# Performance work log

Hardware: AMD Instinct MI355X
Metric: run time of the kernel (lower is better)

The kernel has to match this reference:

```python
import jax, jax.numpy as jnp
from jax import lax
import numpy as np

NPOINT = 1024
RADII = (0.1, 0.2, 0.4)
NSAMPLES = (16, 32, 64)
MLPS = ((64, 64, 128), (128, 128, 256), (128, 128, 256))
IN_CH = 64  # 3 (xyz) + 61 (point features)
EPS = 1e-5


def setup_inputs() -> dict:
    key = jax.random.key(0)
    ks = jax.random.split(key, 64)
    inp = {
        "xyz": jax.random.normal(ks[0], (8, 3, 16384), dtype=jnp.float32),
        "points": jax.random.normal(ks[1], (8, 61, 16384), dtype=jnp.float32),
    }
    ki = 2
    for i, mlp in enumerate(MLPS):
        last = IN_CH
        for j, out_ch in enumerate(mlp):
            inp[f"w{i}{j}"] = jax.random.normal(ks[ki], (out_ch, last), dtype=jnp.float32) * 0.05
            inp[f"b{i}{j}"] = jnp.zeros((out_ch,), dtype=jnp.float32)
            inp[f"g{i}{j}"] = jnp.ones((out_ch,), dtype=jnp.float32)
            inp[f"bt{i}{j}"] = jnp.zeros((out_ch,), dtype=jnp.float32)
            last = out_ch
            ki += 1
    return inp


def square_distance(src, dst):
    # src [B,S,3], dst [B,N,3] -> [B,S,N]
    d = -2.0 * jnp.einsum("bsc,bnc->bsn", src, dst)
    d = d + jnp.sum(src * src, -1)[:, :, None]
    d = d + jnp.sum(dst * dst, -1)[:, None, :]
    return d


def farthest_point_sample(xyz, npoint):
    # xyz [B,N,3] -> idx [B,npoint]; deterministic start at index 0
    B, N, _ = xyz.shape
    def step(carry, _):
        distance, farthest = carry
        centroid = jnp.take_along_axis(xyz, farthest[:, None, None], axis=1)  # [B,1,3]
        dist = jnp.sum((xyz - centroid) ** 2, axis=-1)  # [B,N]
        distance = jnp.minimum(distance, dist)
        return (distance, jnp.argmax(distance, axis=-1).astype(jnp.int32)), farthest
    init = (jnp.full((B, N), 1e10, dtype=xyz.dtype), jnp.zeros((B,), dtype=jnp.int32))
    _, idxs = lax.scan(step, init, None, length=npoint)
    return idxs.T  # [B,npoint]


def gather_points(p, idx):
    # p [B,N,C], idx [B,...] -> [B,...,C]
    B = p.shape[0]
    flat = idx.reshape(B, -1)
    g = jnp.take_along_axis(p, flat[:, :, None], axis=1)
    return g.reshape(idx.shape + (p.shape[-1],))


def query_ball_points(radius, nsample, xyz, new_xyz):
    # xyz [B,N,3], new_xyz [B,S,3] -> idx [B,S,nsample]
    B, N, _ = xyz.shape
    d = square_distance(new_xyz, xyz)  # [B,S,N]
    idx = jnp.broadcast_to(jnp.arange(N, dtype=jnp.int32), d.shape)
    idx = jnp.where(d > radius * radius, N, idx)
    idx = jnp.sort(idx, axis=-1)[:, :, :nsample]
    first = idx[:, :, :1]
    return jnp.where(idx == N, first, idx)


def _forward(xyz, points, params):
    xyz_t = jnp.transpose(xyz, (0, 2, 1))       # [B,N,3]
    pts_t = jnp.transpose(points, (0, 2, 1))    # [B,N,D]
    B, N, _ = xyz_t.shape
    fps_idx = farthest_point_sample(xyz_t, NPOINT)
    new_xyz = gather_points(xyz_t, fps_idx)     # [B,S,3]
    feats = []
    for i, (radius, K) in enumerate(zip(RADII, NSAMPLES)):
        gidx = query_ball_points(radius, K, xyz_t, new_xyz)      # [B,S,K]
        grouped_xyz = gather_points(xyz_t, gidx) - new_xyz[:, :, None, :]
        grouped_pts = gather_points(pts_t, gidx)
        x = jnp.concatenate([grouped_xyz, grouped_pts], axis=-1)  # [B,S,K,IN_CH]
        for (w, b, g, bt) in params[i]:
            x = jnp.einsum("bskc,oc->bsko", x, w) + b  # 1x1 conv
            mean = jnp.mean(x, axis=(0, 1, 2))
            var = jnp.var(x, axis=(0, 1, 2))
            x = jax.nn.relu(g * (x - mean) * lax.rsqrt(var + EPS) + bt)
        feats.append(jnp.max(x, axis=2))  # [B,S,Cout]
    new_points = jnp.transpose(jnp.concatenate(feats, axis=-1), (0, 2, 1))  # [B,640,S]
    return jnp.transpose(new_xyz, (0, 2, 1)), new_points


def reference(xyz, points,
              w00, b00, g00, bt00, w01, b01, g01, bt01, w02, b02, g02, bt02,
              w10, b10, g10, bt10, w11, b11, g11, bt11, w12, b12, g12, bt12,
              w20, b20, g20, bt20, w21, b21, g21, bt21, w22, b22, g22, bt22):
    params = [
        [(w00, b00, g00, bt00), (w01, b01, g01, bt01), (w02, b02, g02, bt02)],
        [(w10, b10, g10, bt10), (w11, b11, g11, bt11), (w12, b12, g12, bt12)],
        [(w20, b20, g20, bt20), (w21, b21, g21, bt21), (w22, b22, g22, bt22)],
    ]
    return _forward(xyz, points, params)
```

## Files before the change

kernel.cpp:

```cpp
#include <hip/hip_runtime.h>
#include <stdint.h>

#define BB 8
#define NN 16384
#define SS 1024

typedef unsigned short u16;
typedef float f32x4 __attribute__((ext_vector_type(4)));
typedef short short8v __attribute__((ext_vector_type(8)));
typedef unsigned short us4 __attribute__((ext_vector_type(4)));
typedef unsigned short us8 __attribute__((ext_vector_type(8)));

static __device__ __forceinline__ float bf2f(u16 u){
    union { uint32_t u; float f; } v; v.u = ((uint32_t)u) << 16; return v.f;
}
static __device__ __forceinline__ u16 f2bf(float f){
    union { float f; uint32_t u; } v; v.f = f;
    return (u16)((v.u + 0x7FFFu + ((v.u >> 16) & 1u)) >> 16);
}
static constexpr int cmax2(int a, int b){ return a > b ? a : b; }

#define LP 12288
#define SM_FPS (LP*3*4 + SS*4 + 8)

__global__ __launch_bounds__(1024) void pre_kernel(
        const float* __restrict__ xyz, const float* __restrict__ pts,
        float* __restrict__ ptsT, float* __restrict__ q, float* __restrict__ out_xyz,
        const float* __restrict__ w0, const float* __restrict__ w1, const float* __restrict__ w2,
        const float* __restrict__ w3, const float* __restrict__ w4, const float* __restrict__ w5,
        const float* __restrict__ w6, const float* __restrict__ w7, const float* __restrict__ w8,
        u16* __restrict__ wbf0, u16* __restrict__ wbf1, u16* __restrict__ wbf2){
#pragma clang fp contract(off)
    __shared__ __align__(16) char smem_raw[SM_FPS];
    int t = threadIdx.x;

    if (blockIdx.x >= 8){
        int bx = blockIdx.x - 8;
        if (bx < 2048){
            float (*tile)[65] = (float (*)[65])smem_raw;
            int b = bx >> 8;
            int n0 = (bx & 255) * 64;
            int ln = t & 63, cr = t >> 6;
            for (int c = cr; c < 64; c += 16){
                float v;
                if (c < 3) v = xyz[((size_t)b*3 + c)*NN + n0 + ln];
                else       v = pts[((size_t)b*61 + (c-3))*NN + n0 + ln];
                tile[ln][c] = v;
            }
            __syncthreads();
            int lc = t & 63, nr = t >> 6;
            for (int n = nr; n < 64; n += 16){
                ptsT[((size_t)b*NN + n0 + n)*64 + lc] = tile[n][lc];
            }
        } else {
            int br = bx - 2048;
            const float* A; const float* B; const float* C; u16* out; int na, nb2, nc;
            if (br == 0){ A=w0; na=4096;  B=w1; nb2=4096;  C=w2; nc=8192;  out=wbf0; }
            else if (br == 1){ A=w3; na=8192; B=w4; nb2=16384; C=w5; nc=32768; out=wbf1; }
            else { A=w6; na=8192; B=w7; nb2=16384; C=w8; nc=32768; out=wbf2; }
            int tot = na + nb2 + nc;
            for (int i = t; i < tot; i += 1024){
                float v;
                if (i < na) v = A[i];
                else if (i < na+nb2) v = B[i-na];
                else v = C[i-na-nb2];
                out[i] = f2bf(v);
            }
        }
        return;
    }

    float* lx = (float*)smem_raw;
    float* ly = lx + LP;
    float* lz = ly + LP;
    int*  hist = (int*)(lz + LP);
    unsigned long long* slotp = (unsigned long long*)(hist + SS);
    int b = blockIdx.x;
    const float* xb = xyz + (size_t)b*3*NN;
    float px[16], py[16], pz[16], dd[16];
#pragma unroll
    for (int j=0;j<16;++j){
        int n = t + j*1024;
        px[j] = xb[n];
        py[j] = xb[NN+n];
        pz[j] = xb[2*NN+n];
        dd[j] = 1e10f;
    }
#pragma unroll
    for (int j=0;j<16;++j){
        asm volatile("" : "+v"(px[j]), "+v"(py[j]), "+v"(pz[j]));
    }
    for (int idx = t; idx < LP; idx += 1024){
        lx[idx] = xb[idx];
        ly[idx] = xb[NN+idx];
        lz[idx] = xb[2*NN+idx];
    }
    if (t == 0) *slotp = 0ull;
    __syncthreads();

    int lane = t & 63;
    int far = 0;
    float cx = xb[0], cy = xb[NN], cz = xb[2*NN];
    for (int it=0; it<SS; ++it){
        if (t==0) hist[it] = far;
#pragma unroll
        for (int j=0;j<16;++j){
            float dx = px[j]-cx, dy = py[j]-cy, dz = pz[j]-cz;
            float d = dx*dx + dy*dy;
            d = d + dz*dz;
            dd[j] = fminf(dd[j], d);
        }
        float m01 = fmaxf(dd[0], dd[1]),  m23 = fmaxf(dd[2], dd[3]);
        float m45 = fmaxf(dd[4], dd[5]),  m67 = fmaxf(dd[6], dd[7]);
        float m89 = fmaxf(dd[8], dd[9]),  mab = fmaxf(dd[10], dd[11]);
        float mcd = fmaxf(dd[12], dd[13]), mef = fmaxf(dd[14], dd[15]);
        float ma = fmaxf(fmaxf(m01, m23), fmaxf(m45, m67));
        float mb = fmaxf(fmaxf(m89, mab), fmaxf(mcd, mef));
        float mx = fmaxf(ma, mb);
        int bj = 0;
#pragma unroll
        for (int j=15; j>=0; --j){
            if (dd[j] == mx) bj = j;
        }
        int bn = t + (bj << 10);
        unsigned long long pk = ((unsigned long long)(unsigned)(it+1) << 46)
                              | ((unsigned long long)__float_as_uint(mx) << 14)
                              | (unsigned long long)(unsigned)(16383 - bn);
#pragma unroll
        for (int off=32; off>0; off>>=1){
            unsigned long long o = __shfl_down(pk, off);
            pk = (o > pk) ? o : pk;
        }
        if (lane == 0) atomicMax(slotp, pk);
        __syncthreads();
        unsigned long long win = *slotp;
        far = 16383 - (int)(win & 0x3FFFull);
        if (far < LP){
            cx = lx[far]; cy = ly[far]; cz = lz[far];
        } else {
            cx = xb[far]; cy = xb[NN+far]; cz = xb[2*NN+far];
        }
    }
    __syncthreads();
    {
        int s = t;
        int fidx = hist[s];
        float vx, vy, vz;
        if (fidx < LP){ vx = lx[fidx]; vy = ly[fidx]; vz = lz[fidx]; }
        else { vx = xb[fidx]; vy = xb[NN+fidx]; vz = xb[2*NN+fidx]; }
        int gi = b*SS + s;
        q[gi*3+0] = vx; q[gi*3+1] = vy; q[gi*3+2] = vz;
        out_xyz[((size_t)b*3+0)*SS + s] = vx;
        out_xyz[((size_t)b*3+1)*SS + s] = vy;
        out_xyz[((size_t)b*3+2)*SS + s] = vz;
    }
}

__global__ __launch_bounds__(256) void ballquery_kernel(const float* __restrict__ xyz, const float* __restrict__ q,
        int* __restrict__ idx0, int* __restrict__ idx1, int* __restrict__ idx2,
        float r2a, float r2b, float r2c){
#pragma clang fp contract(off)
    __shared__ int lds[4][112];
    int t = threadIdx.x;
    int w = t >> 6, lane = t & 63;
    int qi = blockIdx.x*4 + w;
    int b = qi >> 10;
    const float* xb = xyz + (size_t)b*3*NN;
    float qx = q[qi*3], qy = q[qi*3+1], qz = q[qi*3+2];
    float qn = qx*qx + qy*qy; qn = qn + qz*qz;
    int* l0 = lds[w];
    int* l1 = l0 + 16;
    int* l2 = l0 + 48;
    l0[lane] = 0;
    if (lane < 48) l0[64+lane] = 0;
    int c0=0, c1=0, c2=0;
    uint64_t below = (1ull << lane) - 1ull;
    for (int ch=0; ch<256; ++ch){
        int n = ch*64 + lane;
        float x = xb[n], y = xb[NN+n], z = xb[2*NN+n];
        float dn = x*x + y*y; dn = dn + z*z;
        float dot = qx*x + qy*y; dot = dot + qz*z;
        float d = -2.0f*dot + qn;
        d = d + dn;
        bool o0 = d <= r2a, o1 = d <= r2b, o2 = d <= r2c;
        uint64_t m0 = __ballot(o0), m1 = __ballot(o1), m2 = __ballot(o2);
        if (c0 < 16){
            int p = c0 + (int)__popcll(m0 & below);
            if (o0 && p < 16) l0[p] = n;
            c0 += (int)__popcll(m0); if (c0 > 16) c0 = 16;
        }
        if (c1 < 32){
            int p = c1 + (int)__popcll(m1 & below);
            if (o1 && p < 32) l1[p] = n;
            c1 += (int)__popcll(m1); if (c1 > 32) c1 = 32;
        }
        if (c2 < 64){
            int p = c2 + (int)__popcll(m2 & below);
            if (o2 && p < 64) l2[p] = n;
            c2 += (int)__popcll(m2); if (c2 > 64) c2 = 64;
        }
        if (c0>=16 && c1>=32 && c2>=64) break;
    }
    __syncthreads();
    int f0 = l0[0], f1 = l1[0], f2 = l2[0];
    if (lane >= c0 && lane < 16) l0[lane] = f0;
    if (lane >= c1 && lane < 32) l1[lane] = f1;
    if (lane >= c2)              l2[lane] = f2;
    __syncthreads();
    if (lane < 16) idx0[(size_t)qi*16 + lane] = l0[lane];
    if (lane < 32) idx1[(size_t)qi*32 + lane] = l1[lane];
    idx2[(size_t)qi*64 + lane] = l2[lane];
}


template<int CC, int OH>
__device__ __forceinline__ void load_W_frags(const u16* __restrict__ Wb,
                                             short8v (&wf)[CC/32][OH/64],
                                             int l, int w, int hoff){
    int rl = l & 15, kg = l >> 4;
#pragma unroll
    for (int ks=0; ks<CC/32; ++ks)
#pragma unroll
    for (int tc=0; tc<OH/64; ++tc){
        int col = hoff + w*(OH/4) + tc*16 + rl;
        wf[ks][tc] = *(const short8v*)(Wb + (size_t)col*CC + ks*32 + kg*8);
    }
}

template<int K>
__device__ __forceinline__ void stage_A_gather(const float* __restrict__ ptsT, const float* __restrict__ q,
                                               const int* __restrict__ gidx, int m0, int t, char* __restrict__ As){
    int r = t >> 2, q4 = t & 3;
    int m = m0 + r;
    int idx = gidx[m];
    int bs = m / K;
    int b = bs >> 10;
    const float* base = ptsT + ((size_t)b*NN + idx)*64;
    float qx=0.f, qy=0.f, qz=0.f;
    if (q4 == 0){ qx = q[bs*3]; qy = q[bs*3+1]; qz = q[bs*3+2]; }
    int rx = (r & 7) << 4;
#pragma unroll
    for (int ii=0; ii<4; ++ii){
        int c0 = q4*16 + ii*4;
        float4 v = *(const float4*)(base + c0);
        if (q4==0 && ii==0){ v.x -= qx; v.y -= qy; v.z -= qz; }
        us4 u;
        u[0]=f2bf(v.x); u[1]=f2bf(v.y); u[2]=f2bf(v.z); u[3]=f2bf(v.w);
        *(us4*)(As + r*128 + ((c0*2) ^ rx)) = u;
    }
}

template<int OP>
__device__ __forceinline__ void stage_A_z(const u16* __restrict__ zbuf, int m0,
                                          const float* __restrict__ sc, const float* __restrict__ sh,
                                          int t, char* __restrict__ As){
    constexpr int CQ = OP/4;
    for (int s = t; s < 64*CQ; s += 256){
        int r = s / CQ, cq = s - r*CQ;
        us4 zv = *(const us4*)&zbuf[((size_t)(m0+r))*OP + cq*4];
        int c = cq*4;
        us4 u;
        u[0] = f2bf(fmaxf(0.f, bf2f(zv[0])*sc[c+0] + sh[c+0]));
        u[1] = f2bf(fmaxf(0.f, bf2f(zv[1])*sc[c+1] + sh[c+1]));
        u[2] = f2bf(fmaxf(0.f, bf2f(zv[2])*sc[c+2] + sh[c+2]));
        u[3] = f2bf(fmaxf(0.f, bf2f(zv[3])*sc[c+3] + sh[c+3]));
        *(us4*)(As + r*(OP*2) + ((cq*8) ^ ((r&7)<<4))) = u;
    }
}

template<int CC, int OH>
__device__ __forceinline__ void mfma_gemm_v2(const char* __restrict__ As,
                                             const short8v (&wf)[CC/32][OH/64],
                                             f32x4 (&acc)[4][OH/64], int l){
    constexpr int CCB = CC*2;
    int rl = l & 15, kg = l >> 4;
    const char* ap = As + rl*CCB;
    int axor = (rl & 7) << 4;
#pragma unroll
    for (int ks=0; ks<CC/32; ++ks){
        int karg = ((ks<<6) | (kg<<4)) ^ axor;
        short8v a0 = *(const short8v*)(ap + 0*16*CCB + karg);
        short8v a1 = *(const short8v*)(ap + 1*16*CCB + karg);
        short8v a2 = *(const short8v*)(ap + 2*16*CCB + karg);
        short8v a3 = *(const short8v*)(ap + 3*16*CCB + karg);
#pragma unroll
        for (int tc=0; tc<OH/64; ++tc){
            acc[0][tc] = __builtin_amdgcn_mfma_f32_16x16x32_bf16(a0, wf[ks][tc], acc[0][tc], 0,0,0);
            acc[1][tc] = __builtin_amdgcn_mfma_f32_16x16x32_bf16(a1, wf[ks][tc], acc[1][tc], 0,0,0);
            acc[2][tc] = __builtin_amdgcn_mfma_f32_16x16x32_bf16(a2, wf[ks][tc], acc[2][tc], 0,0,0);
            acc[3][tc] = __builtin_amdgcn_mfma_f32_16x16x32_bf16(a3, wf[ks][tc], acc[3][tc], 0,0,0);
        }
    }
}

template<int OH>
__device__ __forceinline__ void bias_mfma(f32x4 (&acc)[4][OH/64], const float* __restrict__ bsrc,
                                          int l, int w, int coff){
#pragma unroll
    for (int tc=0; tc<OH/64; ++tc){
        float bb = bsrc[coff + w*(OH/4) + tc*16 + (l&15)];
#pragma unroll
        for (int tr=0; tr<4; ++tr)
#pragma unroll
        for (int e=0; e<4; ++e) acc[tr][tc][e] += bb;
    }
}

template<int OH, int OT>
__device__ __forceinline__ void zstore_mfma(f32x4 (&acc)[4][OH/64], u16* __restrict__ zbuf,
                                            int m0, int l, int w, int coff){
#pragma unroll
    for (int tr=0; tr<4; ++tr)
#pragma unroll
    for (int e=0; e<4; ++e){
        int row = tr*16 + (l>>4)*4 + e;
#pragma unroll
        for (int tc=0; tc<OH/64; ++tc){
            int c = coff + w*(OH/4) + tc*16 + (l&15);
            zbuf[((size_t)(m0+row))*OT + c] = f2bf(acc[tr][tc][e]);
        }
    }
}

template<int OH, int OT, int K, bool EXT>
__device__ __forceinline__ void stats_mfma(f32x4 (&acc)[4][OH/64], int l, int w, int m0, int blk, int coff,
    float* __restrict__ pS, float* __restrict__ pQ,
    float* __restrict__ gmax, float* __restrict__ gmin){
#pragma unroll
    for (int tc=0; tc<OH/64; ++tc){
        float s1 = 0.f, s2 = 0.f;
        float mxr[4], mnr[4];
#pragma unroll
        for (int tr=0; tr<4; ++tr){
            float v0=acc[tr][tc][0], v1=acc[tr][tc][1], v2=acc[tr][tc][2], v3=acc[tr][tc][3];
            s1 += (v0+v1)+(v2+v3);
            s2 += (v0*v0+v1*v1)+(v2*v2+v3*v3);
            if (EXT){
                mxr[tr] = fmaxf(fmaxf(v0,v1),fmaxf(v2,v3));
                mnr[tr] = fminf(fminf(v0,v1),fminf(v2,v3));
            }
        }
        s1 += __shfl_xor(s1,16); s1 += __shfl_xor(s1,32);
        s2 += __shfl_xor(s2,16); s2 += __shfl_xor(s2,32);
        if (EXT){
#pragma unroll
            for (int tr=0; tr<4; ++tr){
                mxr[tr] = fmaxf(mxr[tr], __shfl_xor(mxr[tr],16));
                mxr[tr] = fmaxf(mxr[tr], __shfl_xor(mxr[tr],32));
                mnr[tr] = fminf(mnr[tr], __shfl_xor(mnr[tr],16));
                mnr[tr] = fminf(mnr[tr], __shfl_xor(mnr[tr],32));
            }
        }
        if (l < 16){
            int c = coff + w*(OH/4) + tc*16 + l;
            pS[(size_t)blk*OT + c] = s1;
            pQ[(size_t)blk*OT + c] = s2;
            if (EXT){
                constexpr int G = 64/K, WG = K/16;
#pragma unroll
                for (int g=0; g<G; ++g){
                    float M1 = mxr[g*WG], M2 = mnr[g*WG];
#pragma unroll
                    for (int ww=1; ww<WG; ++ww){
                        M1 = fmaxf(M1, mxr[g*WG+ww]);
                        M2 = fminf(M2, mnr[g*WG+ww]);
                    }
                    gmax[(size_t)(m0/K + g)*OT + c] = M1;
                    gmin[(size_t)(m0/K + g)*OT + c] = M2;
                }
            }
        }
    }
}

template<int OH>
__device__ __forceinline__ void act_to_As_mfma(f32x4 (&acc)[4][OH/64], const float* __restrict__ bsrc,
    const float* __restrict__ sc, const float* __restrict__ sh, int l, int w, char* __restrict__ As){
#pragma unroll
    for (int tc=0; tc<OH/64; ++tc){
        int c = w*(OH/4) + tc*16 + (l&15);
        float bb = bsrc[c], scv = sc[c], shv = sh[c];
#pragma unroll
        for (int tr=0; tr<4; ++tr)
#pragma unroll
        for (int e=0; e<4; ++e){
            int row = tr*16 + (l>>4)*4 + e;
            float vv = fmaxf(0.f, (acc[tr][tc][e]+bb)*scv + shv);
            *(u16*)(As + row*(OH*2) + ((2*c) ^ ((row&7)<<4))) = f2bf(vv);
        }
    }
}

template<int PHASE, int K, int O1, int O2, int O3>
__global__ __launch_bounds__(256) void fused_mlp(
    const float* __restrict__ ptsT, const float* __restrict__ q, const int* __restrict__ gidx,
    const u16* __restrict__ Wb1, const float* __restrict__ b1,
    const u16* __restrict__ Wb2, const float* __restrict__ b2,
    const u16* __restrict__ Wb3, const float* __restrict__ b3,
    const float* __restrict__ sc1, const float* __restrict__ sh1,
    const float* __restrict__ sc2, const float* __restrict__ sh2,
    float* __restrict__ pS, float* __restrict__ pQ,
    float* __restrict__ gmax, float* __restrict__ gmin,
    u16* __restrict__ zbuf)
{
    constexpr int OH3 = (O3 > 128) ? 128 : O3;
    constexpr int AMX = (PHASE==1) ? 64 : (PHASE==2 ? O1 : (PHASE==3 ? cmax2(O1,O2) : O2));
    __shared__ __align__(16) char As[64*AMX*2];
    int t = threadIdx.x, l = t & 63, w = t >> 6;
    int m0 = blockIdx.x * 64;

    if constexpr (PHASE == 1){
        stage_A_gather<K>(ptsT, q, gidx, m0, t, As);
        short8v wf[2][O1/64];
        load_W_frags<64,O1>(Wb1, wf, l, w, 0);
        __syncthreads();
        f32x4 acc[4][O1/64] = {};
        mfma_gemm_v2<64,O1>(As, wf, acc, l);
        bias_mfma<O1>(acc, b1, l, w, 0);
        if (zbuf) zstore_mfma<O1,O1>(acc, zbuf, m0, l, w, 0);
        stats_mfma<O1,O1,K,false>(acc, l, w, m0, blockIdx.x, 0, pS,pQ,gmax,gmin);
        return;
    }

    if constexpr (PHASE == 2){
        if (zbuf){
            stage_A_z<O1>(zbuf, m0, sc1, sh1, t, As);
        } else {
            stage_A_gather<K>(ptsT, q, gidx, m0, t, As);
            short8v wf1[2][O1/64];
            load_W_frags<64,O1>(Wb1, wf1, l, w, 0);
            __syncthreads();
            f32x4 acc1[4][O1/64] = {};
            mfma_gemm_v2<64,O1>(As, wf1, acc1, l);
            __syncthreads();
            act_to_As_mfma<O1>(acc1, b1, sc1, sh1, l, w, As);
        }
        short8v wf[O1/32][O2/64];
        load_W_frags<O1,O2>(Wb2, wf, l, w, 0);
        __syncthreads();
        f32x4 acc[4][O2/64] = {};
        mfma_gemm_v2<O1,O2>(As, wf, acc, l);
        bias_mfma<O2>(acc, b2, l, w, 0);
        if (zbuf) zstore_mfma<O2,O2>(acc, zbuf, m0, l, w, 0);
        stats_mfma<O2,O2,K,false>(acc, l, w, m0, blockIdx.x, 0, pS,pQ,gmax,gmin);
        return;
    }

    if constexpr (PHASE == 3){
        stage_A_gather<K>(ptsT, q, gidx, m0, t, As);
        short8v wf1[2][O1/64];
        load_W_frags<64,O1>(Wb1, wf1, l, w, 0);
        __syncthreads();
        f32x4 acc1[4][O1/64] = {};
        mfma_gemm_v2<64,O1>(As, wf1, acc1, l);
        __syncthreads();
        act_to_As_mfma<O1>(acc1, b1, sc1, sh1, l, w, As);
        __syncthreads();
        short8v wf2[O1/32][O2/64];
        load_W_frags<O1,O2>(Wb2, wf2, l, w, 0);
        f32x4 acc2[4][O2/64] = {};
        mfma_gemm_v2<O1,O2>(As, wf2, acc2, l);
        __syncthreads();
        act_to_As_mfma<O2>(acc2, b2, sc2, sh2, l, w, As);
    } else {
        stage_A_z<O2>(zbuf, m0, sc2, sh2, t, As);
    }

    __syncthreads();
    constexpr int HH = O3/OH3;
#pragma unroll
    for (int h=0; h<HH; ++h){
        short8v wf[O2/32][OH3/64];
        load_W_frags<O2,OH3>(Wb3, wf, l, w, h*OH3);
        f32x4 acc[4][OH3/64] = {};
        mfma_gemm_v2<O2,OH3>(As, wf, acc, l);
        bias_mfma<OH3>(acc, b3, l, w, h*OH3);
        stats_mfma<OH3,O3,K,true>(acc, l, w, m0, blockIdx.x, h*OH3, pS,pQ,gmax,gmin);
    }
}

__global__ __launch_bounds__(256) void finalize_d_kernel(const float* __restrict__ pS, const float* __restrict__ pQ,
                                      const float* __restrict__ g, const float* __restrict__ bt,
                                      float* __restrict__ sc, float* __restrict__ sh, int nb, double invM){
    __shared__ double red[512];
    int c = blockIdx.x;
    int O = gridDim.x;
    int t = threadIdx.x;
    double S=0.0, Q=0.0;
    for (int v=t; v<nb; v+=256){ S += (double)pS[(size_t)v*O + c]; Q += (double)pQ[(size_t)v*O + c]; }
    red[t]=S; red[256+t]=Q;
    __syncthreads();
    for (int s=128; s>0; s>>=1){
        if (t<s){ red[t]+=red[t+s]; red[256+t]+=red[256+t+s]; }
        __syncthreads();
    }
    if (t==0){
        double mean = red[0]*invM;
        double var  = red[256]*invM - mean*mean;
        double scale = (double)g[c] / sqrt(var + 1e-5);
        sc[c] = (float)scale;
        sh[c] = (float)((double)bt[c] - mean*scale);
    }
}

__global__ void final_out_kernel(const float* __restrict__ gmax, const float* __restrict__ gmin,
                                 const float* __restrict__ sc, const float* __restrict__ sh,
                                 float* __restrict__ outp, int O, int logO, int chbase){
    int gid = blockIdx.x*256 + threadIdx.x;
    int c  = gid & (O-1);
    int bs = gid >> logO;
    int b = bs >> 10, s = bs & 1023;
    float scale = sc[c];
    float v = (scale >= 0.f) ? gmax[gid] : gmin[gid];
    float r = fmaxf(0.f, scale*v + sh[c]);
    outp[((size_t)(b*640 + chbase + c))*SS + s] = r;
}

__global__ void ws_marker_kernel(float* outp, float wsval){ if (threadIdx.x==0) outp[0] = wsval; }

template<int K, int O1, int O2, int O3>
static void run_branch(const float* ptsT, const float* q, const int* gidx,
                       float* pS, float* pQ, float* gmax, float* gmin,
                       float* sc1, float* sh1, float* sc2, float* sh2, float* sc3, float* sh3,
                       u16* z2buf, bool use_z, const u16* wb,
                       void* const* d_in, int wbase, float* np_out, int chbase, hipStream_t stream)
{
    const int M = BB*SS*K;
    const int nb = M/64;
    auto wp = [&](int jl, int which)->const float* { return (const float*)d_in[2 + (wbase+jl)*4 + which]; };
    const double invM = 1.0 / (double)M;
    u16* zb = use_z ? z2buf : (u16*)nullptr;
    const u16* Wb1 = wb;
    const u16* Wb2 = wb + (size_t)O1*64;
    const u16* Wb3 = wb + (size_t)O1*64 + (size_t)O2*O1;

    fused_mlp<1,K,O1,O2,O3><<<nb,256,0,stream>>>(ptsT,q,gidx,
        Wb1,wp(0,1), Wb2,wp(1,1), Wb3,wp(2,1),
        sc1,sh1, sc2,sh2, pS,pQ, gmax,gmin, zb);
    finalize_d_kernel<<<O1,256,0,stream>>>(pS,pQ, wp(0,2), wp(0,3), sc1, sh1, nb, invM);

    fused_mlp<2,K,O1,O2,O3><<<nb,256,0,stream>>>(ptsT,q,gidx,
        Wb1,wp(0,1), Wb2,wp(1,1), Wb3,wp(2,1),
        sc1,sh1, sc2,sh2, pS,pQ, gmax,gmin, zb);
    finalize_d_kernel<<<O2,256,0,stream>>>(pS,pQ, wp(1,2), wp(1,3), sc2, sh2, nb, invM);

    if (use_z){
        fused_mlp<4,K,O1,O2,O3><<<nb,256,0,stream>>>(ptsT,q,gidx,
            Wb1,wp(0,1), Wb2,wp(1,1), Wb3,wp(2,1),
            sc1,sh1, sc2,sh2, pS,pQ, gmax,gmin, z2buf);
    } else {
        fused_mlp<3,K,O1,O2,O3><<<nb,256,0,stream>>>(ptsT,q,gidx,
            Wb1,wp(0,1), Wb2,wp(1,1), Wb3,wp(2,1),
            sc1,sh1, sc2,sh2, pS,pQ, gmax,gmin, nullptr);
    }
    finalize_d_kernel<<<O3,256,0,stream>>>(pS,pQ, wp(2,2), wp(2,3), sc3, sh3, nb, invM);

    final_out_kernel<<<(BB*SS*O3)/256,256,0,stream>>>(gmax,gmin, sc3,sh3, np_out, O3, (O3==256?8:7), chbase);
}

extern "C" void kernel_launch(void* const* d_in, const int* in_sizes, int n_in,
                              void* d_out, int out_size, void* d_ws, size_t ws_size,
                              hipStream_t stream)
{
    const float* xyz = (const float*)d_in[0];
    const float* pts = (const float*)d_in[1];
    float* outp = (float*)d_out;

    char* wsb = (char*)d_ws;
    size_t off = 0;
    auto alloc = [&](size_t bytes) -> void* {
        off = (off + 255) & ~(size_t)255;
        void* p = wsb + off;
        off += bytes;
        return p;
    };
    float* q       = (float*)alloc((size_t)BB*SS*3*4);
    int*   idx0    = (int*)  alloc((size_t)BB*SS*16*4);
    int*   idx1    = (int*)  alloc((size_t)BB*SS*32*4);
    int*   idx2    = (int*)  alloc((size_t)BB*SS*64*4);
    float* ptsT    = (float*)alloc((size_t)BB*NN*64*4);
    float* pS      = (float*)alloc((size_t)8192*256*4);
    float* pQ      = (float*)alloc((size_t)8192*256*4);
    float* gmax    = (float*)alloc((size_t)8192*256*4);
    float* gmin    = (float*)alloc((size_t)8192*256*4);
    float* sc1     = (float*)alloc(256*4);
    float* sh1     = (float*)alloc(256*4);
    float* sc2     = (float*)alloc(256*4);
    float* sh2     = (float*)alloc(256*4);
    float* sc3     = (float*)alloc(256*4);
    float* sh3     = (float*)alloc(256*4);
    u16*   wbf0    = (u16*)  alloc((size_t)16384*2);
    u16*   wbf1    = (u16*)  alloc((size_t)57344*2);
    u16*   wbf2    = (u16*)  alloc((size_t)57344*2);

    if (off > ws_size){
        ws_marker_kernel<<<1,64,0,stream>>>(outp, (float)ws_size);
        return;
    }

    u16* z2buf = (u16*)alloc((size_t)BB*SS*64*128*2);
    bool use_z = (off <= ws_size);

    auto wptr = [&](int layer)->const float* { return (const float*)d_in[2 + layer*4 + 0]; };

    pre_kernel<<<8 + 2048 + 3, 1024, 0, stream>>>(
        xyz, pts, ptsT, q, outp,
        wptr(0), wptr(1), wptr(2), wptr(3), wptr(4), wptr(5), wptr(6), wptr(7), wptr(8),
        wbf0, wbf1, wbf2);

    const float r2a = (float)(0.1*0.1);
    const float r2b = (float)(0.2*0.2);
    const float r2c = (float)(0.4*0.4);
    ballquery_kernel<<<2048, 256, 0, stream>>>(xyz, q, idx0, idx1, idx2, r2a, r2b, r2c);

    float* np_out = outp + (size_t)BB*3*SS;
    run_branch<16, 64, 64,128>(ptsT, q, idx0, pS,pQ, gmax,gmin, sc1,sh1,sc2,sh2,sc3,sh3, z2buf, use_z, wbf0, d_in, 0, np_out,   0, stream);
    run_branch<32,128,128,256>(ptsT, q, idx1, pS,pQ, gmax,gmin, sc1,sh1,sc2,sh2,sc3,sh3, z2buf, use_z, wbf1, d_in, 3, np_out, 128, stream);
    run_branch<64,128,128,256>(ptsT, q, idx2, pS,pQ, gmax,gmin, sc1,sh1,sc2,sh2,sc3,sh3, z2buf, use_z, wbf2, d_in, 6, np_out, 384, stream);

    hipError_t e = hipGetLastError();
    if (e != hipSuccess){
        ws_marker_kernel<<<1,64,0,stream>>>(outp, 1000.0f + (float)(int)e);
    }
}
```

Baseline: 2.756 ms.

## Merge three MSG branches into shared per-phase kernel launches

Gives each of the three scale branches its own stats, max/min and z buffers so that every MLP phase, BN finalize and output step can run as one launch over all branches, with the block index choosing the branch. This removes the serial chain of per-branch launches and the tail effects of small grids, especially for the small first branch. In exchange it needs far more workspace; if that space is not available it falls back to the old per-branch path. The merged kernel also sizes shared memory for the largest branch, which can lower occupancy for the small one.

```diff
diff --git a/kernel.cpp b/kernel.cpp
--- a/kernel.cpp
+++ b/kernel.cpp
@@ -212,7 +212,6 @@
     idx2[(size_t)qi*64 + lane] = l2[lane];
 }
 
-
 template<int CC, int OH>
 __device__ __forceinline__ void load_W_frags(const u16* __restrict__ Wb,
                                              short8v (&wf)[CC/32][OH/64],
@@ -389,6 +388,115 @@
             *(u16*)(As + row*(OH*2) + ((2*c) ^ ((row&7)<<4))) = f2bf(vv);
         }
     }
+}
+
+struct BrP {
+    const int* gidx;
+    const u16 *W1, *W2, *W3;
+    const float *b1, *b2, *b3;
+    const float *sc1, *sh1, *sc2, *sh2;
+    float *pS, *pQ, *gmax, *gmin;
+    u16* zbuf;
+};
+
+template<int PHASE, int K, int O1, int O2, int O3>
+__device__ __forceinline__ void mlp_phase(const float* __restrict__ ptsT, const float* __restrict__ q,
+                                          const BrP& P, int blk, int t, char* As){
+    constexpr int OH3 = (O3 > 128) ? 128 : O3;
+    int l = t & 63, w = t >> 6;
+    int m0 = blk * 64;
+    if constexpr (PHASE == 1){
+        stage_A_gather<K>(ptsT, q, P.gidx, m0, t, As);
+        short8v wf[2][O1/64];
+        load_W_frags<64,O1>(P.W1, wf, l, w, 0);
+        __syncthreads();
+        f32x4 acc[4][O1/64] = {};
+        mfma_gemm_v2<64,O1>(As, wf, acc, l);
+        bias_mfma<O1>(acc, P.b1, l, w, 0);
+        zstore_mfma<O1,O1>(acc, P.zbuf, m0, l, w, 0);
+        stats_mfma<O1,O1,K,false>(acc, l, w, m0, blk, 0, P.pS,P.pQ,P.gmax,P.gmin);
+    } else if constexpr (PHASE == 2){
+        stage_A_z<O1>(P.zbuf, m0, P.sc1, P.sh1, t, As);
+        short8v wf[O1/32][O2/64];
+        load_W_frags<O1,O2>(P.W2, wf, l, w, 0);
+        __syncthreads();
+        f32x4 acc[4][O2/64] = {};
+        mfma_gemm_v2<O1,O2>(As, wf, acc, l);
+        bias_mfma<O2>(acc, P.b2, l, w, 0);
+        zstore_mfma<O2,O2>(acc, P.zbuf, m0, l, w, 0);
+        stats_mfma<O2,O2,K,false>(acc, l, w, m0, blk, 0, P.pS,P.pQ,P.gmax,P.gmin);
+    } else {
+        stage_A_z<O2>(P.zbuf, m0, P.sc2, P.sh2, t, As);
+        __syncthreads();
+        constexpr int HH = O3/OH3;
+#pragma unroll
+        for (int h=0; h<HH; ++h){
+            short8v wf[O2/32][OH3/64];
+            load_W_frags<O2,OH3>(P.W3, wf, l, w, h*OH3);
+            f32x4 acc[4][OH3/64] = {};
+            mfma_gemm_v2<O2,OH3>(As, wf, acc, l);
+            bias_mfma<OH3>(acc, P.b3, l, w, h*OH3);
+            stats_mfma<OH3,O3,K,true>(acc, l, w, m0, blk, h*OH3, P.pS,P.pQ,P.gmax,P.gmin);
+        }
+    }
+}
+
+template<int PHASE>
+__global__ __launch_bounds__(256) void mlp_stage_kernel(const float* __restrict__ ptsT,
+                                                        const float* __restrict__ q,
+                                                        BrP p0, BrP p1, BrP p2){
+    constexpr int AMX = (PHASE==1) ? 64 : 128;
+    __shared__ __align__(16) char As[64*AMX*2];
+    int t = threadIdx.x;
+    int bx = blockIdx.x;
+    if (bx < 8192)        mlp_phase<PHASE,64,128,128,256>(ptsT, q, p2, bx, t, As);
+    else if (bx < 12288)  mlp_phase<PHASE,32,128,128,256>(ptsT, q, p1, bx-8192, t, As);
+    else                  mlp_phase<PHASE,16, 64, 64,128>(ptsT, q, p0, bx-12288, t, As);
+}
+
+struct FinP { const float *pS, *pQ, *g, *bt; float *sc, *sh; int O, nb; double invM; };
+
+__global__ __launch_bounds__(256) void finalize_merged_kernel(FinP f0, FinP f1, FinP f2){
+    __shared__ double red[512];
+    int bx = blockIdx.x;
+    FinP f; int c;
+    if (bx < f2.O){ f = f2; c = bx; }
+    else if (bx < f2.O + f1.O){ f = f1; c = bx - f2.O; }
+    else { f = f0; c = bx - f2.O - f1.O; }
+    int t = threadIdx.x;
+    double S=0.0, Q=0.0;
+    for (int v=t; v<f.nb; v+=256){ S += (double)f.pS[(size_t)v*f.O + c]; Q += (double)f.pQ[(size_t)v*f.O + c]; }
+    red[t]=S; red[256+t]=Q;
+    __syncthreads();
+    for (int s=128; s>0; s>>=1){
+        if (t<s){ red[t]+=red[t+s]; red[256+t]+=red[256+t+s]; }
+        __syncthreads();
+    }
+    if (t==0){
+        double mean = red[0]*f.invM;
+        double var  = red[256]*f.invM - mean*mean;
+        double scale = (double)f.g[c] / sqrt(var + 1e-5);
+        f.sc[c] = (float)scale;
+        f.sh[c] = (float)((double)f.bt[c] - mean*scale);
+    }
+}
+
+struct OutP { const float *gmax, *gmin, *sc, *sh; int O, logO, chbase; };
+
+__global__ void final_out_merged_kernel(OutP o0, OutP o1, OutP o2, float* __restrict__ outp){
+    int bx = blockIdx.x;
+    OutP o; int base;
+    if (bx < 8192){ o = o2; base = bx; }
+    else if (bx < 16384){ o = o1; base = bx - 8192; }
+    else { o = o0; base = bx - 16384; }
+    int gid = base*256 + threadIdx.x;
+    int c  = gid & (o.O-1);
+    int bs = gid >> o.logO;
+    int b = bs >> 10, s = bs & 1023;
+    float scale = o.sc[c];
+    float v = (scale >= 0.f) ? o.gmax[gid] : o.gmin[gid];
+    float r = fmaxf(0.f, scale*v + o.sh[c]);
+    outp[((size_t)(b*640 + o.chbase + c))*SS + s] = r;
 }
 
 template<int PHASE, int K, int O1, int O2, int O3>
@@ -579,33 +687,39 @@
     int*   idx1    = (int*)  alloc((size_t)BB*SS*32*4);
     int*   idx2    = (int*)  alloc((size_t)BB*SS*64*4);
     float* ptsT    = (float*)alloc((size_t)BB*NN*64*4);
-    float* pS      = (float*)alloc((size_t)8192*256*4);
-    float* pQ      = (float*)alloc((size_t)8192*256*4);
-    float* gmax    = (float*)alloc((size_t)8192*256*4);
-    float* gmin    = (float*)alloc((size_t)8192*256*4);
-    float* sc1     = (float*)alloc(256*4);
-    float* sh1     = (float*)alloc(256*4);
-    float* sc2     = (float*)alloc(256*4);
-    float* sh2     = (float*)alloc(256*4);
-    float* sc3     = (float*)alloc(256*4);
-    float* sh3     = (float*)alloc(256*4);
     u16*   wbf0    = (u16*)  alloc((size_t)16384*2);
     u16*   wbf1    = (u16*)  alloc((size_t)57344*2);
     u16*   wbf2    = (u16*)  alloc((size_t)57344*2);
+    float* scsh    = (float*)alloc((size_t)3*6*256*4);
+    size_t off_common = off;
 
     if (off > ws_size){
         ws_marker_kernel<<<1,64,0,stream>>>(outp, (float)ws_size);
         return;
     }
 
-    u16* z2buf = (u16*)alloc((size_t)BB*SS*64*128*2);
-    bool use_z = (off <= ws_size);
-
-    auto wptr = [&](int layer)->const float* { return (const float*)d_in[2 + layer*4 + 0]; };
+    float* pS0 = (float*)alloc((size_t)2048*128*4);
+    float* pS1 = (float*)alloc((size_t)4096*256*4);
+    float* pS2 = (float*)alloc((size_t)8192*256*4);
+    float* pQ0 = (float*)alloc((size_t)2048*128*4);
+    float* pQ1 = (float*)alloc((size_t)4096*256*4);
+    float* pQ2 = (float*)alloc((size_t)8192*256*4);
+    float* gx0 = (float*)alloc((size_t)8192*128*4);
+    float* gx1 = (float*)alloc((size_t)8192*256*4);
+    float* gx2 = (float*)alloc((size_t)8192*256*4);
+    float* gn0 = (float*)alloc((size_t)8192*128*4);
+    float* gn1 = (float*)alloc((size_t)8192*256*4);
+    float* gn2 = (float*)alloc((size_t)8192*256*4);
+    u16*   zb0 = (u16*)  alloc((size_t)131072*64*2);
+    u16*   zb1 = (u16*)  alloc((size_t)262144*128*2);
+    u16*   zb2 = (u16*)  alloc((size_t)524288*128*2);
+    bool merged = (off <= ws_size);
+
+    auto wptr = [&](int layer, int which)->const float* { return (const float*)d_in[2 + layer*4 + which]; };
 
     pre_kernel<<<8 + 2048 + 3, 1024, 0, stream>>>(
         xyz, pts, ptsT, q, outp,
-        wptr(0), wptr(1), wptr(2), wptr(3), wptr(4), wptr(5), wptr(6), wptr(7), wptr(8),
+        wptr(0,0), wptr(1,0), wptr(2,0), wptr(3,0), wptr(4,0), wptr(5,0), wptr(6,0), wptr(7,0), wptr(8,0),
         wbf0, wbf1, wbf2);
 
     const float r2a = (float)(0.1*0.1);
@@ -614,9 +728,74 @@
     ballquery_kernel<<<2048, 256, 0, stream>>>(xyz, q, idx0, idx1, idx2, r2a, r2b, r2c);
 
     float* np_out = outp + (size_t)BB*3*SS;
-    run_branch<16, 64, 64,128>(ptsT, q, idx0, pS,pQ, gmax,gmin, sc1,sh1,sc2,sh2,sc3,sh3, z2buf, use_z, wbf0, d_in, 0, np_out,   0, stream);
-    run_branch<32,128,128,256>(ptsT, q, idx1, pS,pQ, gmax,gmin, sc1,sh1,sc2,sh2,sc3,sh3, z2buf, use_z, wbf1, d_in, 3, np_out, 128, stream);
-    run_branch<64,128,128,256>(ptsT, q, idx2, pS,pQ, gmax,gmin, sc1,sh1,sc2,sh2,sc3,sh3, z2buf, use_z, wbf2, d_in, 6, np_out, 384, stream);
+
+    if (merged){
+        auto SC = [&](int br, int slot)->float* { return scsh + ((size_t)br*6 + slot)*256; };
+        BrP P[3];
+        const u16* wb[3] = { wbf0, wbf1, wbf2 };
+        const int O1s[3] = {64,128,128}, O2s[3] = {64,128,128}, O3s[3] = {128,256,256};
+        const int* gidxs[3] = { idx0, idx1, idx2 };
+        float* pSs[3] = {pS0,pS1,pS2}; float* pQs[3] = {pQ0,pQ1,pQ2};
+        float* gxs[3] = {gx0,gx1,gx2}; float* gns[3] = {gn0,gn1,gn2};
+        u16* zbs[3] = {zb0,zb1,zb2};
+        for (int br=0; br<3; ++br){
+            int wbase = br*3;
+            P[br].gidx = gidxs[br];
+            P[br].W1 = wb[br];
+            P[br].W2 = wb[br] + (size_t)O1s[br]*64;
+            P[br].W3 = wb[br] + (size_t)O1s[br]*64 + (size_t)O2s[br]*O1s[br];
+            P[br].b1 = wptr(wbase+0,1); P[br].b2 = wptr(wbase+1,1); P[br].b3 = wptr(wbase+2,1);
+            P[br].sc1 = SC(br,0); P[br].sh1 = SC(br,1);
+            P[br].sc2 = SC(br,2); P[br].sh2 = SC(br,3);
+            P[br].pS = pSs[br]; P[br].pQ = pQs[br];
+            P[br].gmax = gxs[br]; P[br].gmin = gns[br];
+            P[br].zbuf = zbs[br];
+        }
+        const int nbs[3] = {2048, 4096, 8192};
+        const double invMs[3] = {1.0/131072.0, 1.0/262144.0, 1.0/524288.0};
+        auto mkFin = [&](int br, int layer, int O, float* sc, float* sh)->FinP{
+            FinP f; f.pS = pSs[br]; f.pQ = pQs[br];
+            f.g = wptr(br*3+layer,2); f.bt = wptr(br*3+layer,3);
+            f.sc = sc; f.sh = sh; f.O = O; f.nb = nbs[br]; f.invM = invMs[br];
+            return f;
+        };
+
+        mlp_stage_kernel<1><<<14336,256,0,stream>>>(ptsT, q, P[0], P[1], P[2]);
+        finalize_merged_kernel<<<64+128+128,256,0,stream>>>(
+            mkFin(0,0,64,SC(0,0),SC(0,1)), mkFin(1,0,128,SC(1,0),SC(1,1)), mkFin(2,0,128,SC(2,0),SC(2,1)));
+
+        mlp_stage_kernel<2><<<14336,256,0,stream>>>(ptsT, q, P[0], P[1], P[2]);
+        finalize_merged_kernel<<<64+128+128,256,0,stream>>>(
+            mkFin(0,1,64,SC(0,2),SC(0,3)), mkFin(1,1,128,SC(1,2),SC(1,3)), mkFin(2,1,128,SC(2,2),SC(2,3)));
+
+        mlp_stage_kernel<4><<<14336,256,0,stream>>>(ptsT, q, P[0], P[1], P[2]);
+        finalize_merged_kernel<<<128+256+256,256,0,stream>>>(
+            mkFin(0,2,128,SC(0,4),SC(0,5)), mkFin(1,2,256,SC(1,4),SC(1,5)), mkFin(2,2,256,SC(2,4),SC(2,5)));
+
+        OutP o0 = { gx0, gn0, SC(0,4), SC(0,5), 128, 7,   0 };
+        OutP o1 = { gx1, gn1, SC(1,4), SC(1,5), 256, 8, 128 };
+        OutP o2 = { gx2, gn2, SC(2,4), SC(2,5), 256, 8, 384 };
+        final_out_merged_kernel<<<8192+8192+4096,256,0,stream>>>(o0, o1, o2, np_out);
+    } else {
+        off = off_common;
+        float* pS   = (float*)alloc((size_t)8192*256*4);
+        float* pQ   = (float*)alloc((size_t)8192*256*4);
+        float* gmax = (float*)alloc((size_t)8192*256*4);
+        float* gmin = (float*)alloc((size_t)8192*256*4);
+        if (off > ws_size){
+            ws_marker_kernel<<<1,64,0,stream>>>(outp, (float)ws_size);
+            return;
+        }
+        u16* z2buf = (u16*)alloc((size_t)BB*SS*64*128*2);
+        bool use_z = (off <= ws_size);
+        float* sc1 = scsh+0*256; float* sh1 = scsh+1*256;
+        float* sc2 = scsh+2*256; float* sh2 = scsh+3*256;
+        float* sc3 = scsh+4*256; float* sh3 = scsh+5*256;
+
+        run_branch<16, 64, 64,128>(ptsT, q, idx0, pS,pQ, gmax,gmin, sc1,sh1,sc2,sh2,sc3,sh3, z2buf, use_z, wbf0, d_in, 0, np_out,   0, stream);
+        run_branch<32,128,128,256>(ptsT, q, idx1, pS,pQ, gmax,gmin, sc1,sh1,sc2,sh2,sc3,sh3, z2buf, use_z, wbf1, d_in, 3, np_out, 128, stream);
+        run_branch<64,128,128,256>(ptsT, q, idx2, pS,pQ, gmax,gmin, sc1,sh1,sc2,sh2,sc3,sh3, z2buf, use_z, wbf2, d_in, 6, np_out, 384, stream);
+    }
 
     hipError_t e = hipGetLastError();
     if (e != hipSuccess){
```

Measured after the change: 2.760 ms. Within noise of the previous version (+0.2%).
